# Optimization experiments

Measured on AMD Instinct MI355X. Metric: run time of the kernel, lower is better.

## Reference

```python
import jax, jax.numpy as jnp
import numpy as np

N, H = 65536, 256
RHO_REF = 1000.0
MOMENTUM_W, CONTINUITY_W = 1.0, 10.0


def setup_inputs() -> dict:
    key = jax.random.key(0)
    ks = jax.random.split(key, 6)
    sc = lambda k, shape, fan_in: jax.random.normal(k, shape, jnp.float32) * (1.0 / fan_in) ** 0.5
    return {
        "sample_points": jax.random.normal(ks[0], (N, 3), jnp.float32),
        "sample_times": jax.random.uniform(ks[1], (N, 1), jnp.float32),
        "viscosity": jax.random.uniform(ks[2], (N,), jnp.float32) * 1e-3 + 1e-6,
        "W1": sc(ks[3], (4, H), 4),
        "b1": jnp.zeros((H,), jnp.float32),
        "W2": sc(ks[4], (H, H), H),
        "b2": jnp.zeros((H,), jnp.float32),
        "W3": sc(ks[5], (H, 5), H),
        "b3": jnp.zeros((5,), jnp.float32),
    }


def reference(sample_points, sample_times, viscosity, W1, b1, W2, b2, W3, b3):
    gravity = jnp.array([0.0, -9.81, 0.0], dtype=sample_points.dtype)

    def mlp(z):  # z: (4,) = (x, y, zcoord, t) -> (5,) = (ux, uy, uz, p, rho_raw)
        h = jnp.tanh(z @ W1 + b1)
        h = jnp.tanh(h @ W2 + b2)
        return h @ W3 + b3

    def up_fn(z):  # (ux, uy, uz, p)
        return mlp(z)[:4]

    def u_fn(z):  # (ux, uy, uz)
        return mlp(z)[:3]

    def per_point(z):
        out = mlp(z)
        u = out[:3]
        rho = RHO_REF * (1.0 + 0.1 * jnp.tanh(out[4]))
        J = jax.jacfwd(up_fn)(z)                      # (4,4): d[u,p]/d[x,y,z,t]
        Hs = jax.jacfwd(jax.jacfwd(u_fn))(z)          # (3,4,4): second derivs of u
        lap = Hs[:, 0, 0] + Hs[:, 1, 1] + Hs[:, 2, 2]  # (3,) spatial Laplacian of u
        return u, rho, J, lap

    z = jnp.concatenate([sample_points, sample_times], axis=1)  # (N,4)
    u, rho, J, lap = jax.vmap(per_point)(z)

    du_dt = J[:, :3, 3]                                # (N,3)
    conv = jnp.einsum('nj,nij->ni', u, J[:, :3, :3])   # (u . grad) u
    grad_p = J[:, 3, :3]                               # (N,3)
    R = du_dt + conv + grad_p / rho[:, None] - viscosity[:, None] * lap - gravity[None, :]
    R_cont = J[:, 0, 0] + J[:, 1, 1] + J[:, 2, 2]      # div u

    momentum_loss = (R ** 2).mean(axis=0).sum()
    continuity_loss = (R_cont ** 2).mean()
    total = MOMENTUM_W * momentum_loss + CONTINUITY_W * continuity_loss
    return jnp.stack([total, momentum_loss, continuity_loss])
```

## Files before the change

### kernel.cpp

```cpp
#include <hip/hip_runtime.h>


#define NPTS 65536
#define BP   8
#define NBLK (NPTS / BP)
#define KPADB 264
#define W3T_OFF 135168
#define PART_OFF 143360

typedef float f32x4 __attribute__((ext_vector_type(4)));

static __device__ __forceinline__ unsigned cvtpk_fp8(float lo, float hi){
  unsigned r = 0;
  asm("v_cvt_pk_fp8_f32 %0, %1, %2" : "+v"(r) : "v"(lo), "v"(hi));
  return r;
}
static __device__ __forceinline__ float fast_tanh(float x){
  float e = __builtin_amdgcn_exp2f(x * 2.8853900817779268f);
  return 1.f - 2.f * __builtin_amdgcn_rcpf(e + 1.f);
}

__global__ void prep_w2t(const float* __restrict__ W2, unsigned char* __restrict__ w2t){
  int kp = blockIdx.x, j = threadIdx.x;
  float lo = W2[(2*kp    )*256 + j];
  float hi = W2[(2*kp + 1)*256 + j];
  *(unsigned short*)(w2t + j*KPADB + 2*kp) = (unsigned short)cvtpk_fp8(lo, hi);
}
__global__ void prep_w3t(const float* __restrict__ W3, unsigned char* __restrict__ w3t){
  int n = blockIdx.x, k2 = threadIdx.x * 2;
  float lo = (n < 5) ? W3[k2*5 + n]       : 0.f;
  float hi = (n < 5) ? W3[(k2+1)*5 + n]   : 0.f;
  *(unsigned short*)(w3t + n*256 + k2) = (unsigned short)cvtpk_fp8(lo, hi);
}

__launch_bounds__(256, 4)
__global__ void ns_main(const float* __restrict__ pts, const float* __restrict__ times,
                        const float* __restrict__ visc,
                        const float* __restrict__ W1, const float* __restrict__ b1,
                        const float* __restrict__ b2, const float* __restrict__ b3,
                        const unsigned char* __restrict__ w2t,
                        const unsigned char* __restrict__ w3t,
                        float* __restrict__ parts){
  __shared__ __align__(16) unsigned char sA[64 * 256];
  __shared__ float red[8];

  const int t   = threadIdx.x;
  const int blk = blockIdx.x;

  {
    int p  = t >> 5;
    int jo = (t & 31) << 3;
    int n  = blk * BP + p;
    float z0 = pts[n*3+0], z1 = pts[n*3+1], z2 = pts[n*3+2], z3 = times[n];
    float w0v[8], w1v[8], w2v[8], w3v[8], bv[8];
    *(float4*)(w0v)   = *(const float4*)(W1 + jo);
    *(float4*)(w0v+4) = *(const float4*)(W1 + jo + 4);
    *(float4*)(w1v)   = *(const float4*)(W1 + 256 + jo);
    *(float4*)(w1v+4) = *(const float4*)(W1 + 256 + jo + 4);
    *(float4*)(w2v)   = *(const float4*)(W1 + 512 + jo);
    *(float4*)(w2v+4) = *(const float4*)(W1 + 512 + jo + 4);
    *(float4*)(w3v)   = *(const float4*)(W1 + 768 + jo);
    *(float4*)(w3v+4) = *(const float4*)(W1 + 768 + jo + 4);
    *(float4*)(bv)    = *(const float4*)(b1 + jo);
    *(float4*)(bv+4)  = *(const float4*)(b1 + jo + 4);
    float th[8], sg[8], m2[8];
    #pragma unroll
    for (int jj = 0; jj < 8; ++jj){
      float a  = bv[jj] + z0*w0v[jj] + z1*w1v[jj] + z2*w2v[jj] + z3*w3v[jj];
      float h  = fast_tanh(a);
      th[jj] = h; sg[jj] = 1.f - h*h; m2[jj] = -2.f*h*sg[jj];
    }
    #pragma unroll
    for (int c = 0; c < 8; ++c){
      float x[8];
      #pragma unroll
      for (int jj = 0; jj < 8; ++jj){
        float v;
        if      (c == 0) v = th[jj];
        else if (c == 1) v = sg[jj]*w0v[jj];
        else if (c == 2) v = sg[jj]*w1v[jj];
        else if (c == 3) v = sg[jj]*w2v[jj];
        else if (c == 4) v = sg[jj]*w3v[jj];
        else if (c == 5) v = m2[jj]*w0v[jj]*w0v[jj];
        else if (c == 6) v = m2[jj]*w1v[jj]*w1v[jj];
        else             v = m2[jj]*w2v[jj]*w2v[jj];
        x[jj] = v;
      }
      int row = ((p & 4) << 3) + ((c & 4) << 2) + ((p & 3) << 2) + (c & 3);
      int off = row*256 + (jo ^ ((row & 7) << 3));
      uint2 v2;
      v2.x = cvtpk_fp8(x[0], x[1]) | (cvtpk_fp8(x[2], x[3]) << 16);
      v2.y = cvtpk_fp8(x[4], x[5]) | (cvtpk_fp8(x[6], x[7]) << 16);
      *(uint2*)(sA + off) = v2;
    }
  }
  __syncthreads();

  const int wid = t >> 6, lane = t & 63;
  const int g = lane >> 4, r16 = lane & 15;
  const int xorv = (r16 & 7) << 3;

  f32x4 acc[4][4];
  #pragma unroll
  for (int a = 0; a < 4; ++a)
    #pragma unroll
    for (int b = 0; b < 4; ++b)
      acc[a][b] = (f32x4){0.f, 0.f, 0.f, 0.f};

  {
    int abase = r16*256;
    const unsigned char* bptr[4];
    #pragma unroll
    for (int nt = 0; nt < 4; ++nt)
      bptr[nt] = w2t + (wid*64 + nt*16 + r16)*KPADB + g*8;
    #pragma unroll
    for (int ks = 0; ks < 8; ++ks){
      int k0 = ks * 32;
      int X  = (k0 + (g << 3)) ^ xorv;
      long af[4], bfr[4];
      #pragma unroll
      for (int mt = 0; mt < 4; ++mt)
        af[mt] = *(const long*)(sA + abase + mt*4096 + X);
      #pragma unroll
      for (int nt = 0; nt < 4; ++nt)
        bfr[nt] = *(const long*)(bptr[nt] + k0);
      __builtin_amdgcn_s_setprio(1);
      #pragma unroll
      for (int mt = 0; mt < 4; ++mt)
        #pragma unroll
        for (int nt = 0; nt < 4; ++nt)
          acc[mt][nt] = __builtin_amdgcn_mfma_f32_16x16x32_fp8_fp8(af[mt], bfr[nt], acc[mt][nt], 0, 0, 0);
      __builtin_amdgcn_s_setprio(0);
    }
  }
  __syncthreads();

  {
    float b2c[4];
    #pragma unroll
    for (int nt = 0; nt < 4; ++nt) b2c[nt] = b2[wid*64 + nt*16 + r16];
    int wadr[4][4];
    #pragma unroll
    for (int nt = 0; nt < 4; ++nt){
      int colb = wid*64 + nt*16 + r16;
      #pragma unroll
      for (int c3 = 0; c3 < 4; ++c3)
        wadr[nt][c3] = (g*4 + c3)*256 + (colb ^ ((((g & 1) << 2) + c3) << 3));
    }
    #pragma unroll
    for (int pr = 0; pr < 2; ++pr){
      #pragma unroll
      for (int nt = 0; nt < 4; ++nt){
        f32x4 v = acc[2*pr][nt];
        f32x4 w = acc[2*pr+1][nt];
        float gv = fast_tanh(v[0] + b2c[nt]);
        float s2 = 1.f - gv*gv;
        float t2 = -2.f * gv * s2;
        float r0 = gv,      r1 = s2*v[1], r2 = s2*v[2], r3 = s2*v[3];
        float r4 = s2*w[0];
        float r5 = fmaf(t2*v[1], v[1], s2*w[1]);
        float r6 = fmaf(t2*v[2], v[2], s2*w[2]);
        float r7 = fmaf(t2*v[3], v[3], s2*w[3]);
        unsigned u;
        u = cvtpk_fp8(r0, r4);
        *(unsigned char*)(sA + wadr[nt][0] + pr*8192)        = (unsigned char)u;
        *(unsigned char*)(sA + wadr[nt][0] + pr*8192 + 4096) = (unsigned char)(u >> 8);
        u = cvtpk_fp8(r1, r5);
        *(unsigned char*)(sA + wadr[nt][1] + pr*8192)        = (unsigned char)u;
        *(unsigned char*)(sA + wadr[nt][1] + pr*8192 + 4096) = (unsigned char)(u >> 8);
        u = cvtpk_fp8(r2, r6);
        *(unsigned char*)(sA + wadr[nt][2] + pr*8192)        = (unsigned char)u;
        *(unsigned char*)(sA + wadr[nt][2] + pr*8192 + 4096) = (unsigned char)(u >> 8);
        u = cvtpk_fp8(r3, r7);
        *(unsigned char*)(sA + wadr[nt][3] + pr*8192)        = (unsigned char)u;
        *(unsigned char*)(sA + wadr[nt][3] + pr*8192 + 4096) = (unsigned char)(u >> 8);
      }
    }
  }
  __syncthreads();

  float accM = 0.f, accC = 0.f;
  {
    const int ptL  = 2*wid + ((r16 >> 2) & 1);
    const int jrow = ((ptL & 4) << 3) + ((ptL & 3) << 2) + (r16 & 3) + ((r16 >> 3) << 4);
    const int g3off = jrow * 256;
    const int g3sw  = (jrow & 7) << 3;
    const unsigned char* w3p = w3t + r16*256 + g*8;
    const float b3v = (r16 < 5) ? b3[r16] : 0.f;

    f32x4 a3 = (f32x4){0.f, 0.f, 0.f, 0.f};
    #pragma unroll
    for (int ks = 0; ks < 8; ++ks){
      int k0 = ks * 32;
      int X  = (k0 + (g << 3)) ^ g3sw;
      long av  = *(const long*)(sA + g3off + X);
      long bv3 = *(const long*)(w3p + k0);
      a3 = __builtin_amdgcn_mfma_f32_16x16x32_fp8_fp8(av, bv3, a3, 0, 0, 0);
    }
    float o4 = __shfl_xor(a3[0], 32, 64);
    float o5 = __shfl_xor(a3[1], 32, 64);
    float o6 = __shfl_xor(a3[2], 32, 64);
    float o7 = __shfl_xor(a3[3], 32, 64);
    float o0 = a3[0] + b3v, o1 = a3[1], o2 = a3[2], o3 = a3[3];
    int sl = lane & 16;
    float u0 = __shfl(o0, sl | 0, 64);
    float u1 = __shfl(o0, sl | 1, 64);
    float u2 = __shfl(o0, sl | 2, 64);
    float rhoA = __shfl(o0, sl | 4, 64);
    float gpx = __shfl(o1, sl | 3, 64);
    float gpy = __shfl(o2, sl | 3, 64);
    float gpz = __shfl(o3, sl | 3, 64);
    float c00 = __shfl(o1, sl | 0, 64);
    float c11 = __shfl(o2, sl | 1, 64);
    float c22 = __shfl(o3, sl | 2, 64);
    float rho = 1000.f * (1.f + 0.1f * fast_tanh(rhoA));
    float rr  = __builtin_amdgcn_rcpf(rho);
    float vis = visc[blk*BP + ptL];
    float lap = o5 + o6 + o7;
    float cv  = u0*o1 + u1*o2 + u2*o3;
    float gp  = (r16 == 0) ? gpx : ((r16 == 1) ? gpy : gpz);
    float R   = o4 + cv + gp*rr - vis*lap + ((r16 == 1) ? 9.81f : 0.f);
    if (lane < 32){
      if (r16 < 3) accM += R*R;
      else if (r16 == 3){ float Rc = c00 + c11 + c22; accC += Rc*Rc; }
    }
  }

  #pragma unroll
  for (int off = 1; off < 64; off <<= 1){
    accM += __shfl_xor(accM, off, 64);
    accC += __shfl_xor(accC, off, 64);
  }
  if (lane == 0){ red[wid*2] = accM; red[wid*2+1] = accC; }
  __syncthreads();
  if (t == 0){
    float m = red[0] + red[2] + red[4] + red[6];
    float c = red[1] + red[3] + red[5] + red[7];
    float2 pr; pr.x = m; pr.y = c;
    *(float2*)(parts + blk*2) = pr;
  }
}

__global__ void ns_reduce(const float* __restrict__ parts, float* __restrict__ out){
  int t = threadIdx.x;
  float a = 0.f, b = 0.f;
  for (int i = t; i < NBLK; i += 256){ a += parts[2*i]; b += parts[2*i + 1]; }
  #pragma unroll
  for (int off = 32; off; off >>= 1){
    a += __shfl_down(a, off, 64);
    b += __shfl_down(b, off, 64);
  }
  __shared__ float sa[4], sb[4];
  int wid = t >> 6, lane = t & 63;
  if (lane == 0){ sa[wid] = a; sb[wid] = b; }
  __syncthreads();
  if (t == 0){
    float A = sa[0] + sa[1] + sa[2] + sa[3];
    float B = sb[0] + sb[1] + sb[2] + sb[3];
    float mom  = A / (float)NPTS;
    float cont = B / (float)NPTS;
    out[0] = mom + 10.f * cont;
    out[1] = mom;
    out[2] = cont;
  }
}

extern "C" void kernel_launch(void* const* d_in, const int* in_sizes, int n_in,
                              void* d_out, int out_size, void* d_ws, size_t ws_size,
                              hipStream_t stream) {
  const float* pts   = (const float*)d_in[0];
  const float* times = (const float*)d_in[1];
  const float* visc  = (const float*)d_in[2];
  const float* W1    = (const float*)d_in[3];
  const float* b1    = (const float*)d_in[4];
  const float* W2    = (const float*)d_in[5];
  const float* b2    = (const float*)d_in[6];
  const float* W3    = (const float*)d_in[7];
  const float* b3    = (const float*)d_in[8];
  float* out = (float*)d_out;

  unsigned char* w2t = (unsigned char*)d_ws;
  unsigned char* w3t = (unsigned char*)d_ws + W3T_OFF;
  float* parts       = (float*)((char*)d_ws + PART_OFF);

  prep_w2t<<<128, 256, 0, stream>>>(W2, w2t);
  prep_w3t<<<16, 128, 0, stream>>>(W3, w3t);
  ns_main<<<NBLK, 256, 0, stream>>>(pts, times, visc, W1, b1, b2, b3, w2t, w3t, parts);
  ns_reduce<<<1, 256, 0, stream>>>(parts, out);
}
```

Baseline: 120.2 us.

## Halve points per block to shrink LDS and accumulators, restructure layer-3 epilogue

Each block now handles 4 points instead of 8, so the shared activation tile halves to 8 KB and each wave keeps 2x4 MFMA accumulator tiles instead of 4x4. The launch bound rises to 5 waves per SIMD to allow more resident blocks. The output layer is computed by a single wave with two MFMA chains, which removes the cross-wave shared reduction and one barrier. The trade-off is twice as many blocks, so every W2 fragment is reloaded from global/L2 for half as many points, and three of the four waves sit idle during the final stage.

```diff
diff --git a/kernel.cpp b/kernel.cpp
--- a/kernel.cpp
+++ b/kernel.cpp
@@ -2,7 +2,7 @@
 
 
 #define NPTS 65536
-#define BP   8
+#define BP   4
 #define NBLK (NPTS / BP)
 #define KPADB 264
 #define W3T_OFF 135168
@@ -33,7 +33,7 @@
   *(unsigned short*)(w3t + n*256 + k2) = (unsigned short)cvtpk_fp8(lo, hi);
 }
 
-__launch_bounds__(256, 4)
+__launch_bounds__(256, 5)
 __global__ void ns_main(const float* __restrict__ pts, const float* __restrict__ times,
                         const float* __restrict__ visc,
                         const float* __restrict__ W1, const float* __restrict__ b1,
@@ -41,68 +41,61 @@
                         const unsigned char* __restrict__ w2t,
                         const unsigned char* __restrict__ w3t,
                         float* __restrict__ parts){
-  __shared__ __align__(16) unsigned char sA[64 * 256];
-  __shared__ float red[8];
+  __shared__ __align__(16) unsigned char sA[32 * 256];
 
   const int t   = threadIdx.x;
   const int blk = blockIdx.x;
 
   {
-    int p  = t >> 5;
-    int jo = (t & 31) << 3;
+    int p  = t >> 6;
+    int jo = (t & 63) << 2;
     int n  = blk * BP + p;
     float z0 = pts[n*3+0], z1 = pts[n*3+1], z2 = pts[n*3+2], z3 = times[n];
-    float w0v[8], w1v[8], w2v[8], w3v[8], bv[8];
-    *(float4*)(w0v)   = *(const float4*)(W1 + jo);
-    *(float4*)(w0v+4) = *(const float4*)(W1 + jo + 4);
-    *(float4*)(w1v)   = *(const float4*)(W1 + 256 + jo);
-    *(float4*)(w1v+4) = *(const float4*)(W1 + 256 + jo + 4);
-    *(float4*)(w2v)   = *(const float4*)(W1 + 512 + jo);
-    *(float4*)(w2v+4) = *(const float4*)(W1 + 512 + jo + 4);
-    *(float4*)(w3v)   = *(const float4*)(W1 + 768 + jo);
-    *(float4*)(w3v+4) = *(const float4*)(W1 + 768 + jo + 4);
-    *(float4*)(bv)    = *(const float4*)(b1 + jo);
-    *(float4*)(bv+4)  = *(const float4*)(b1 + jo + 4);
-    float th[8], sg[8], m2[8];
-    #pragma unroll
-    for (int jj = 0; jj < 8; ++jj){
-      float a  = bv[jj] + z0*w0v[jj] + z1*w1v[jj] + z2*w2v[jj] + z3*w3v[jj];
-      float h  = fast_tanh(a);
+    float4 wa  = *(const float4*)(W1 + jo);
+    float4 wb  = *(const float4*)(W1 + 256 + jo);
+    float4 wcv = *(const float4*)(W1 + 512 + jo);
+    float4 wd  = *(const float4*)(W1 + 768 + jo);
+    float4 bb  = *(const float4*)(b1 + jo);
+    float th[4], sg[4], m2[4];
+    #pragma unroll
+    for (int jj = 0; jj < 4; ++jj){
+      float a = (&bb.x)[jj] + z0*(&wa.x)[jj] + z1*(&wb.x)[jj]
+                            + z2*(&wcv.x)[jj] + z3*(&wd.x)[jj];
+      float h = fast_tanh(a);
       th[jj] = h; sg[jj] = 1.f - h*h; m2[jj] = -2.f*h*sg[jj];
     }
     #pragma unroll
     for (int c = 0; c < 8; ++c){
-      float x[8];
+      float x[4];
       #pragma unroll
-      for (int jj = 0; jj < 8; ++jj){
+      for (int jj = 0; jj < 4; ++jj){
+        float w0 = (&wa.x)[jj], w1 = (&wb.x)[jj], w2 = (&wcv.x)[jj];
         float v;
         if      (c == 0) v = th[jj];
-        else if (c == 1) v = sg[jj]*w0v[jj];
-        else if (c == 2) v = sg[jj]*w1v[jj];
-        else if (c == 3) v = sg[jj]*w2v[jj];
-        else if (c == 4) v = sg[jj]*w3v[jj];
-        else if (c == 5) v = m2[jj]*w0v[jj]*w0v[jj];
-        else if (c == 6) v = m2[jj]*w1v[jj]*w1v[jj];
-        else             v = m2[jj]*w2v[jj]*w2v[jj];
+        else if (c == 1) v = sg[jj]*w0;
+        else if (c == 2) v = sg[jj]*w1;
+        else if (c == 3) v = sg[jj]*w2;
+        else if (c == 4) v = sg[jj]*(&wd.x)[jj];
+        else if (c == 5) v = m2[jj]*w0*w0;
+        else if (c == 6) v = m2[jj]*w1*w1;
+        else             v = m2[jj]*w2*w2;
         x[jj] = v;
       }
-      int row = ((p & 4) << 3) + ((c & 4) << 2) + ((p & 3) << 2) + (c & 3);
-      int off = row*256 + (jo ^ ((row & 7) << 3));
-      uint2 v2;
-      v2.x = cvtpk_fp8(x[0], x[1]) | (cvtpk_fp8(x[2], x[3]) << 16);
-      v2.y = cvtpk_fp8(x[4], x[5]) | (cvtpk_fp8(x[6], x[7]) << 16);
-      *(uint2*)(sA + off) = v2;
+      int row = ((c & 4) << 2) + (p << 2) + (c & 3);
+      int off = row*256 + (jo ^ ((row & 15) << 3));
+      unsigned v32 = cvtpk_fp8(x[0], x[1]) | (cvtpk_fp8(x[2], x[3]) << 16);
+      *(unsigned*)(sA + off) = v32;
     }
   }
   __syncthreads();
 
   const int wid = t >> 6, lane = t & 63;
   const int g = lane >> 4, r16 = lane & 15;
-  const int xorv = (r16 & 7) << 3;
-
-  f32x4 acc[4][4];
+  const int rsw = r16 << 3;
+
+  f32x4 acc[2][4];
   #pragma unroll
-  for (int a = 0; a < 4; ++a)
+  for (int a = 0; a < 2; ++a)
     #pragma unroll
     for (int b = 0; b < 4; ++b)
       acc[a][b] = (f32x4){0.f, 0.f, 0.f, 0.f};
@@ -116,20 +109,22 @@
     #pragma unroll
     for (int ks = 0; ks < 8; ++ks){
       int k0 = ks * 32;
-      int X  = (k0 + (g << 3)) ^ xorv;
-      long af[4], bfr[4];
-      #pragma unroll
-      for (int mt = 0; mt < 4; ++mt)
-        af[mt] = *(const long*)(sA + abase + mt*4096 + X);
-      #pragma unroll
-      for (int nt = 0; nt < 4; ++nt)
-        bfr[nt] = *(const long*)(bptr[nt] + k0);
+      int X  = (k0 + (g << 3)) ^ rsw;
+      long af0 = *(const long*)(sA + abase + X);
+      long af1 = *(const long*)(sA + abase + 4096 + X);
+      long b0  = *(const long*)(bptr[0] + k0);
+      long b1f = *(const long*)(bptr[1] + k0);
+      long b2f = *(const long*)(bptr[2] + k0);
+      long b3f = *(const long*)(bptr[3] + k0);
       __builtin_amdgcn_s_setprio(1);
-      #pragma unroll
-      for (int mt = 0; mt < 4; ++mt)
-        #pragma unroll
-        for (int nt = 0; nt < 4; ++nt)
-          acc[mt][nt] = __builtin_amdgcn_mfma_f32_16x16x32_fp8_fp8(af[mt], bfr[nt], acc[mt][nt], 0, 0, 0);
+      acc[0][0] = __builtin_amdgcn_mfma_f32_16x16x32_fp8_fp8(af0, b0,  acc[0][0], 0, 0, 0);
+      acc[1][0] = __builtin_amdgcn_mfma_f32_16x16x32_fp8_fp8(af1, b0,  acc[1][0], 0, 0, 0);
+      acc[0][1] = __builtin_amdgcn_mfma_f32_16x16x32_fp8_fp8(af0, b1f, acc[0][1], 0, 0, 0);
+      acc[1][1] = __builtin_amdgcn_mfma_f32_16x16x32_fp8_fp8(af1, b1f, acc[1][1], 0, 0, 0);
+      acc[0][2] = __builtin_amdgcn_mfma_f32_16x16x32_fp8_fp8(af0, b2f, acc[0][2], 0, 0, 0);
+      acc[1][2] = __builtin_amdgcn_mfma_f32_16x16x32_fp8_fp8(af1, b2f, acc[1][2], 0, 0, 0);
+      acc[0][3] = __builtin_amdgcn_mfma_f32_16x16x32_fp8_fp8(af0, b3f, acc[0][3], 0, 0, 0);
+      acc[1][3] = __builtin_amdgcn_mfma_f32_16x16x32_fp8_fp8(af1, b3f, acc[1][3], 0, 0, 0);
       __builtin_amdgcn_s_setprio(0);
     }
   }
@@ -145,99 +140,84 @@
       int colb = wid*64 + nt*16 + r16;
       #pragma unroll
       for (int c3 = 0; c3 < 4; ++c3)
-        wadr[nt][c3] = (g*4 + c3)*256 + (colb ^ ((((g & 1) << 2) + c3) << 3));
-    }
-    #pragma unroll
-    for (int pr = 0; pr < 2; ++pr){
-      #pragma unroll
-      for (int nt = 0; nt < 4; ++nt){
-        f32x4 v = acc[2*pr][nt];
-        f32x4 w = acc[2*pr+1][nt];
-        float gv = fast_tanh(v[0] + b2c[nt]);
-        float s2 = 1.f - gv*gv;
-        float t2 = -2.f * gv * s2;
-        float r0 = gv,      r1 = s2*v[1], r2 = s2*v[2], r3 = s2*v[3];
-        float r4 = s2*w[0];
-        float r5 = fmaf(t2*v[1], v[1], s2*w[1]);
-        float r6 = fmaf(t2*v[2], v[2], s2*w[2]);
-        float r7 = fmaf(t2*v[3], v[3], s2*w[3]);
-        unsigned u;
-        u = cvtpk_fp8(r0, r4);
-        *(unsigned char*)(sA + wadr[nt][0] + pr*8192)        = (unsigned char)u;
-        *(unsigned char*)(sA + wadr[nt][0] + pr*8192 + 4096) = (unsigned char)(u >> 8);
-        u = cvtpk_fp8(r1, r5);
-        *(unsigned char*)(sA + wadr[nt][1] + pr*8192)        = (unsigned char)u;
-        *(unsigned char*)(sA + wadr[nt][1] + pr*8192 + 4096) = (unsigned char)(u >> 8);
-        u = cvtpk_fp8(r2, r6);
-        *(unsigned char*)(sA + wadr[nt][2] + pr*8192)        = (unsigned char)u;
-        *(unsigned char*)(sA + wadr[nt][2] + pr*8192 + 4096) = (unsigned char)(u >> 8);
-        u = cvtpk_fp8(r3, r7);
-        *(unsigned char*)(sA + wadr[nt][3] + pr*8192)        = (unsigned char)u;
-        *(unsigned char*)(sA + wadr[nt][3] + pr*8192 + 4096) = (unsigned char)(u >> 8);
-      }
-    }
-  }
-  __syncthreads();
-
-  float accM = 0.f, accC = 0.f;
-  {
-    const int ptL  = 2*wid + ((r16 >> 2) & 1);
-    const int jrow = ((ptL & 4) << 3) + ((ptL & 3) << 2) + (r16 & 3) + ((r16 >> 3) << 4);
-    const int g3off = jrow * 256;
-    const int g3sw  = (jrow & 7) << 3;
+        wadr[nt][c3] = (g*4 + c3)*256 + (colb ^ ((g*4 + c3) << 3));
+    }
+    #pragma unroll
+    for (int nt = 0; nt < 4; ++nt){
+      f32x4 v = acc[0][nt];
+      f32x4 w = acc[1][nt];
+      float gv = fast_tanh(v[0] + b2c[nt]);
+      float s2 = 1.f - gv*gv;
+      float t2 = -2.f * gv * s2;
+      float r0 = gv,      r1 = s2*v[1], r2 = s2*v[2], r3 = s2*v[3];
+      float r4 = s2*w[0];
+      float r5 = fmaf(t2*v[1], v[1], s2*w[1]);
+      float r6 = fmaf(t2*v[2], v[2], s2*w[2]);
+      float r7 = fmaf(t2*v[3], v[3], s2*w[3]);
+      unsigned u;
+      u = cvtpk_fp8(r0, r4);
+      *(unsigned char*)(sA + wadr[nt][0])        = (unsigned char)u;
+      *(unsigned char*)(sA + wadr[nt][0] + 4096) = (unsigned char)(u >> 8);
+      u = cvtpk_fp8(r1, r5);
+      *(unsigned char*)(sA + wadr[nt][1])        = (unsigned char)u;
+      *(unsigned char*)(sA + wadr[nt][1] + 4096) = (unsigned char)(u >> 8);
+      u = cvtpk_fp8(r2, r6);
+      *(unsigned char*)(sA + wadr[nt][2])        = (unsigned char)u;
+      *(unsigned char*)(sA + wadr[nt][2] + 4096) = (unsigned char)(u >> 8);
+      u = cvtpk_fp8(r3, r7);
+      *(unsigned char*)(sA + wadr[nt][3])        = (unsigned char)u;
+      *(unsigned char*)(sA + wadr[nt][3] + 4096) = (unsigned char)(u >> 8);
+    }
+  }
+  __syncthreads();
+
+  if (wid == 0){
     const unsigned char* w3p = w3t + r16*256 + g*8;
-    const float b3v = (r16 < 5) ? b3[r16] : 0.f;
-
-    f32x4 a3 = (f32x4){0.f, 0.f, 0.f, 0.f};
+    f32x4 a3a = (f32x4){0.f, 0.f, 0.f, 0.f};
+    f32x4 a3b = (f32x4){0.f, 0.f, 0.f, 0.f};
     #pragma unroll
     for (int ks = 0; ks < 8; ++ks){
       int k0 = ks * 32;
-      int X  = (k0 + (g << 3)) ^ g3sw;
-      long av  = *(const long*)(sA + g3off + X);
+      int X  = (k0 + (g << 3)) ^ rsw;
+      long ava = *(const long*)(sA + r16*256 + X);
+      long avb = *(const long*)(sA + r16*256 + 4096 + X);
       long bv3 = *(const long*)(w3p + k0);
-      a3 = __builtin_amdgcn_mfma_f32_16x16x32_fp8_fp8(av, bv3, a3, 0, 0, 0);
-    }
-    float o4 = __shfl_xor(a3[0], 32, 64);
-    float o5 = __shfl_xor(a3[1], 32, 64);
-    float o6 = __shfl_xor(a3[2], 32, 64);
-    float o7 = __shfl_xor(a3[3], 32, 64);
-    float o0 = a3[0] + b3v, o1 = a3[1], o2 = a3[2], o3 = a3[3];
-    int sl = lane & 16;
-    float u0 = __shfl(o0, sl | 0, 64);
-    float u1 = __shfl(o0, sl | 1, 64);
-    float u2 = __shfl(o0, sl | 2, 64);
+      a3a = __builtin_amdgcn_mfma_f32_16x16x32_fp8_fp8(ava, bv3, a3a, 0, 0, 0);
+      a3b = __builtin_amdgcn_mfma_f32_16x16x32_fp8_fp8(avb, bv3, a3b, 0, 0, 0);
+    }
+    float b3v = (r16 < 5) ? b3[r16] : 0.f;
+    float o0 = a3a[0] + b3v;
+    float o1 = a3a[1], o2 = a3a[2], o3 = a3a[3];
+    int sl = lane & 48;
+    float u0   = __shfl(o0, sl | 0, 64);
+    float u1   = __shfl(o0, sl | 1, 64);
+    float u2   = __shfl(o0, sl | 2, 64);
     float rhoA = __shfl(o0, sl | 4, 64);
-    float gpx = __shfl(o1, sl | 3, 64);
-    float gpy = __shfl(o2, sl | 3, 64);
-    float gpz = __shfl(o3, sl | 3, 64);
-    float c00 = __shfl(o1, sl | 0, 64);
-    float c11 = __shfl(o2, sl | 1, 64);
-    float c22 = __shfl(o3, sl | 2, 64);
+    float gpx  = __shfl(o1, sl | 3, 64);
+    float gpy  = __shfl(o2, sl | 3, 64);
+    float gpz  = __shfl(o3, sl | 3, 64);
+    float c00  = __shfl(o1, sl | 0, 64);
+    float c11  = __shfl(o2, sl | 1, 64);
+    float c22  = __shfl(o3, sl | 2, 64);
     float rho = 1000.f * (1.f + 0.1f * fast_tanh(rhoA));
     float rr  = __builtin_amdgcn_rcpf(rho);
-    float vis = visc[blk*BP + ptL];
-    float lap = o5 + o6 + o7;
+    float vis = visc[blk*BP + g];
+    float lap = a3b[1] + a3b[2] + a3b[3];
     float cv  = u0*o1 + u1*o2 + u2*o3;
     float gp  = (r16 == 0) ? gpx : ((r16 == 1) ? gpy : gpz);
-    float R   = o4 + cv + gp*rr - vis*lap + ((r16 == 1) ? 9.81f : 0.f);
-    if (lane < 32){
-      if (r16 < 3) accM += R*R;
-      else if (r16 == 3){ float Rc = c00 + c11 + c22; accC += Rc*Rc; }
-    }
-  }
-
-  #pragma unroll
-  for (int off = 1; off < 64; off <<= 1){
-    accM += __shfl_xor(accM, off, 64);
-    accC += __shfl_xor(accC, off, 64);
-  }
-  if (lane == 0){ red[wid*2] = accM; red[wid*2+1] = accC; }
-  __syncthreads();
-  if (t == 0){
-    float m = red[0] + red[2] + red[4] + red[6];
-    float c = red[1] + red[3] + red[5] + red[7];
-    float2 pr; pr.x = m; pr.y = c;
-    *(float2*)(parts + blk*2) = pr;
+    float R   = a3b[0] + cv + gp*rr - vis*lap + ((r16 == 1) ? 9.81f : 0.f);
+    float accM = (r16 < 3) ? R*R : 0.f;
+    float accC = 0.f;
+    if (r16 == 3){ float Rc = c00 + c11 + c22; accC = Rc*Rc; }
+    #pragma unroll
+    for (int off = 1; off < 64; off <<= 1){
+      accM += __shfl_xor(accM, off, 64);
+      accC += __shfl_xor(accC, off, 64);
+    }
+    if (lane == 0){
+      float2 pr; pr.x = accM; pr.y = accC;
+      *(float2*)(parts + blk*2) = pr;
+    }
   }
 }
 
```

After: 164.3 us. 36.7% more time.
